# Optimization experiments

Measured on AMD Instinct MI355X. Metric: run time of the kernel, lower is better.

## Reference

```python
import jax, jax.numpy as jnp
import numpy as np

SCALE = 64.0   # CosFace scale s
MARGIN = 0.35  # CosFace margin m
EPS = 1e-12


def setup_inputs() -> dict:
    key = jax.random.key(0)
    k1, k2, k3 = jax.random.split(key, 3)
    batch, feat_dim, num_classes = 512, 512, 100000
    return {
        "input": jax.random.normal(k1, (batch, feat_dim), dtype=jnp.float32),
        "label": jax.random.randint(k2, (batch,), 0, num_classes, dtype=jnp.int64),
        "w": jax.random.normal(k3, (feat_dim, num_classes), dtype=jnp.float32),
    }


def reference(input, label, w):
    # L2-normalize features (rows) and class weights (columns), as in _forward_train
    feat_norm = jnp.clip(jnp.linalg.norm(input, axis=1, keepdims=True), EPS, None)
    normed_feat = input / feat_norm                      # [B, D]
    w_norm = jnp.clip(jnp.linalg.norm(w, axis=0, keepdims=True), EPS, None)
    normed_w = w / w_norm                                # [D, C]
    cosine = jnp.clip(normed_feat @ normed_w, -1.0, 1.0)  # [B, C]
    # CosFace margin applied at the true-label position (get_probs_i)
    onehot = jax.nn.one_hot(label, w.shape[1], dtype=cosine.dtype)
    logits = SCALE * (cosine - MARGIN * onehot)          # [B, C]
    # loss = mean(logsumexp over all (sharded) classes - logit at true label)
    lse = jax.nn.logsumexp(logits, axis=1)               # [B]
    x = jnp.take_along_axis(logits, label[:, None], axis=1)[:, 0]  # [B]
    return jnp.mean(lse - x)
```

## Files before the change

### kernel.cpp

```cpp
#include <hip/hip_runtime.h>
#include <hip/hip_bf16.h>
#include <math.h>

#define BDIM 512
#define DDIM 512
#define CDIM 100000
#define NC 64
#define NCHUNK ((CDIM + NC - 1) / NC)

typedef __attribute__((ext_vector_type(8))) short short8;
typedef __attribute__((ext_vector_type(4))) float f32x4;

__device__ __forceinline__ unsigned short f2bf(float f) {
  unsigned int u = __builtin_bit_cast(unsigned int, f);
  u = (u + 0x7FFFu + ((u >> 16) & 1u)) >> 16;
  return (unsigned short)u;
}

__global__ void k_rownorm(const float* __restrict__ x, unsigned short* __restrict__ a) {
  const int b = blockIdx.x;
  const int tid = threadIdx.x;
  const float* row = x + (size_t)b * DDIM;
  float v0 = row[tid], v1 = row[tid + 256];
  float ss = v0 * v0 + v1 * v1;
  #pragma unroll
  for (int m = 1; m < 64; m <<= 1) ss += __shfl_xor(ss, m);
  __shared__ float sred[4];
  __shared__ float sinv;
  if ((tid & 63) == 0) sred[tid >> 6] = ss;
  __syncthreads();
  if (tid == 0) {
    float s = sred[0] + sred[1] + sred[2] + sred[3];
    sinv = 1.f / fmaxf(sqrtf(s), 1e-12f);
  }
  __syncthreads();
  const float inv = sinv;
  a[(size_t)b * DDIM + tid] = f2bf(v0 * inv);
  a[(size_t)b * DDIM + tid + 256] = f2bf(v1 * inv);
}

__global__ __launch_bounds__(512, 4)
void k_main(const unsigned short* __restrict__ a,
            const float* __restrict__ w,
            const long long* __restrict__ label,
            float2* __restrict__ part,
            float* __restrict__ labellogit) {
  __shared__ __align__(16) unsigned short blds[NC][DDIM];
  __shared__ float ssred[8][NC];
  __shared__ float invwn_sh[NC];

  const int t = threadIdx.x;
  const int chunk = blockIdx.x;
  const int c0 = chunk * NC;
  const bool tailblk = (c0 + NC > CDIM);

  const int wave = t >> 6;
  const int lane = t & 63;
  const int lhi = lane >> 4;
  const int llo = lane & 15;

  const int c4 = (t & 15) * 4;
  const int tg = t >> 4;

  float4 p[16];
  if (!tailblk) {
    #pragma unroll
    for (int h = 0; h < 2; h++)
      #pragma unroll
      for (int j = 0; j < 8; j++) {
        const int k = (tg + 32 * h) * 8 + j;
        p[h * 8 + j] = *reinterpret_cast<const float4*>(w + (size_t)k * CDIM + c0 + c4);
      }
  } else {
    #pragma unroll
    for (int h = 0; h < 2; h++)
      #pragma unroll
      for (int j = 0; j < 8; j++) {
        const int k = (tg + 32 * h) * 8 + j;
        #pragma unroll
        for (int cc = 0; cc < 4; cc++)
          p[h * 8 + j][cc] = (c0 + c4 + cc < CDIM) ? w[(size_t)k * CDIM + c0 + c4 + cc] : 0.f;
      }
  }

  float ss0 = 0.f, ss1 = 0.f, ss2 = 0.f, ss3 = 0.f;
  #pragma unroll
  for (int i = 0; i < 16; i++) {
    ss0 += p[i].x * p[i].x; ss1 += p[i].y * p[i].y;
    ss2 += p[i].z * p[i].z; ss3 += p[i].w * p[i].w;
  }

  #pragma unroll
  for (int h = 0; h < 2; h++) {
    #pragma unroll
    for (int cc = 0; cc < 4; cc++) {
      const int c = c4 + cc;
      short8 v;
      #pragma unroll
      for (int j = 0; j < 8; j++) v[j] = (short)f2bf(p[h * 8 + j][cc]);
      *reinterpret_cast<short8*>(&blds[c][((tg + 32 * h) * 8) ^ ((c & 7) << 3)]) = v;
    }
  }

  #pragma unroll
  for (int msk = 16; msk < 64; msk <<= 1) {
    ss0 += __shfl_xor(ss0, msk);
    ss1 += __shfl_xor(ss1, msk);
    ss2 += __shfl_xor(ss2, msk);
    ss3 += __shfl_xor(ss3, msk);
  }
  if (lane < 16) {
    ssred[wave][c4 + 0] = ss0;
    ssred[wave][c4 + 1] = ss1;
    ssred[wave][c4 + 2] = ss2;
    ssred[wave][c4 + 3] = ss3;
  }
  __syncthreads();
  if (t < NC) {
    float s = 0.f;
    #pragma unroll
    for (int i = 0; i < 8; i++) s += ssred[i][t];
    invwn_sh[t] = 1.f / fmaxf(sqrtf(s), 1e-12f);
  }
  __syncthreads();

  f32x4 acc[4][4];
  #pragma unroll
  for (int i = 0; i < 4; i++)
    #pragma unroll
    for (int j = 0; j < 4; j++)
      acc[i][j] = (f32x4){0.f, 0.f, 0.f, 0.f};

  const unsigned short* ab0 = a + (size_t)(wave * 64 + 0 * 16 + llo) * DDIM + (lhi << 3);
  const unsigned short* ab1 = a + (size_t)(wave * 64 + 1 * 16 + llo) * DDIM + (lhi << 3);
  const unsigned short* ab2 = a + (size_t)(wave * 64 + 2 * 16 + llo) * DDIM + (lhi << 3);
  const unsigned short* ab3 = a + (size_t)(wave * 64 + 3 * 16 + llo) * DDIM + (lhi << 3);

  #pragma unroll
  for (int step = 0; step < 16; step++) {
    const int koff = step * 32;
    short8 af[4], bfr[4];
    af[0] = *reinterpret_cast<const short8*>(ab0 + koff);
    af[1] = *reinterpret_cast<const short8*>(ab1 + koff);
    af[2] = *reinterpret_cast<const short8*>(ab2 + koff);
    af[3] = *reinterpret_cast<const short8*>(ab3 + koff);
    #pragma unroll
    for (int cf = 0; cf < 4; cf++) {
      const int c = cf * 16 + llo;
      bfr[cf] = *reinterpret_cast<const short8*>(
          &blds[c][(koff + (lhi << 3)) ^ ((c & 7) << 3)]);
    }
    #pragma unroll
    for (int rf = 0; rf < 4; rf++)
      #pragma unroll
      for (int cf = 0; cf < 4; cf++)
        acc[rf][cf] = __builtin_amdgcn_mfma_f32_16x16x32_bf16(af[rf], bfr[cf], acc[rf][cf], 0, 0, 0);
  }

  #pragma unroll
  for (int rf = 0; rf < 4; rf++) {
    #pragma unroll
    for (int r = 0; r < 4; r++) {
      const int row = wave * 64 + rf * 16 + (lhi << 2) + r;
      const int lab = (int)label[row];
      float vals[4];
      float mloc = -INFINITY;
      #pragma unroll
      for (int cf = 0; cf < 4; cf++) {
        const int cg = c0 + cf * 16 + llo;
        float cs = acc[rf][cf][r] * invwn_sh[cf * 16 + llo];
        cs = fminf(fmaxf(cs, -1.f), 1.f);
        float lg = 64.f * cs;
        if (cg == lab) { lg = 64.f * (cs - 0.35f); labellogit[row] = lg; }
        if (cg >= CDIM) lg = -INFINITY;
        vals[cf] = lg;
        mloc = fmaxf(mloc, lg);
      }
      float m = mloc;
      #pragma unroll
      for (int msk = 1; msk < 16; msk <<= 1) m = fmaxf(m, __shfl_xor(m, msk));
      float s = 0.f;
      #pragma unroll
      for (int cf = 0; cf < 4; cf++) s += __expf(vals[cf] - m);
      #pragma unroll
      for (int msk = 1; msk < 16; msk <<= 1) s += __shfl_xor(s, msk);
      if (llo == 0) part[(size_t)chunk * BDIM + row] = make_float2(m, s);
    }
  }
}

__global__ void k_rowreduce(const float2* __restrict__ part,
                            const float* __restrict__ labellogit,
                            float* __restrict__ rowloss) {
  const int row = blockIdx.x;
  const int tid = threadIdx.x;
  float m = -INFINITY, s = 0.f;
  for (int ch = tid; ch < NCHUNK; ch += 256) {
    float2 p = part[(size_t)ch * BDIM + row];
    float nm = fmaxf(m, p.x);
    s = s * __expf(m - nm) + p.y * __expf(p.x - nm);
    m = nm;
  }
  #pragma unroll
  for (int msk = 1; msk < 64; msk <<= 1) {
    float om = __shfl_xor(m, msk), os = __shfl_xor(s, msk);
    float nm = fmaxf(m, om);
    s = s * __expf(m - nm) + os * __expf(om - nm);
    m = nm;
  }
  __shared__ float sm[4], ssum[4];
  const int wv = tid >> 6, ln = tid & 63;
  if (ln == 0) { sm[wv] = m; ssum[wv] = s; }
  __syncthreads();
  if (tid == 0) {
    float M = sm[0], S = ssum[0];
    #pragma unroll
    for (int i = 1; i < 4; i++) {
      float nm = fmaxf(M, sm[i]);
      S = S * __expf(M - nm) + ssum[i] * __expf(sm[i] - nm);
      M = nm;
    }
    rowloss[row] = M + logf(S) - labellogit[row];
  }
}

__global__ void k_mean(const float* __restrict__ rowloss, float* __restrict__ out) {
  const int tid = threadIdx.x;
  float v = rowloss[tid];
  #pragma unroll
  for (int msk = 1; msk < 64; msk <<= 1) v += __shfl_xor(v, msk);
  __shared__ float sred[8];
  if ((tid & 63) == 0) sred[tid >> 6] = v;
  __syncthreads();
  if (tid == 0) {
    float s = 0.f;
    #pragma unroll
    for (int i = 0; i < 8; i++) s += sred[i];
    out[0] = s / (float)BDIM;
  }
}

extern "C" void kernel_launch(void* const* d_in, const int* in_sizes, int n_in,
                              void* d_out, int out_size, void* d_ws, size_t ws_size,
                              hipStream_t stream) {
  const float* input = (const float*)d_in[0];
  const long long* label = (const long long*)d_in[1];
  const float* w = (const float*)d_in[2];
  float* out = (float*)d_out;

  char* ws = (char*)d_ws;
  unsigned short* a_bf16 = (unsigned short*)ws;
  float2* part = (float2*)(ws + 512 * 1024);
  float* labellogit = (float*)(ws + 512 * 1024 + (size_t)BDIM * NCHUNK * sizeof(float2));
  float* rowloss = labellogit + BDIM;

  k_rownorm<<<BDIM, 256, 0, stream>>>(input, a_bf16);
  k_main<<<NCHUNK, 512, 0, stream>>>(a_bf16, w, label, part, labellogit);
  k_rowreduce<<<BDIM, 256, 0, stream>>>(part, labellogit, rowloss);
  k_mean<<<1, BDIM, 0, stream>>>(rowloss, out);
}
```

Before: 173.1 us.

## Pre-transpose W to bf16 with column norms, then stream tiles via global_load_lds

Adds a separate kernel that reads the fp32 weight matrix once. It transposes it through shared memory into a column-major bf16 copy in workspace and computes the inverse column norms there. The main GEMM kernel no longer converts or reduces fp32 weights. It loads each 64-column tile straight into swizzled LDS with direct global-to-LDS loads and reads the precomputed norms. This removes the strided fp32 loads and conversion from the MFMA kernel, at the cost of an extra bf16 write and re-read of the whole weight matrix and one more launch.

```diff
diff --git a/kernel.cpp b/kernel.cpp
--- a/kernel.cpp
+++ b/kernel.cpp
@@ -7,6 +7,8 @@
 #define CDIM 100000
 #define NC 64
 #define NCHUNK ((CDIM + NC - 1) / NC)
+#define CPAD (NCHUNK * NC)
+#define CTILE 128
 
 typedef __attribute__((ext_vector_type(8))) short short8;
 typedef __attribute__((ext_vector_type(4))) float f32x4;
@@ -15,6 +17,12 @@
   unsigned int u = __builtin_bit_cast(unsigned int, f);
   u = (u + 0x7FFFu + ((u >> 16) & 1u)) >> 16;
   return (unsigned short)u;
+}
+
+__device__ __forceinline__ void gl_lds16(const unsigned short* g, unsigned short* l) {
+  __builtin_amdgcn_global_load_lds(
+      (const __attribute__((address_space(1))) void*)g,
+      (__attribute__((address_space(3))) void*)l, 16, 0, 0);
 }
 
 __global__ void k_rownorm(const float* __restrict__ x, unsigned short* __restrict__ a) {
@@ -39,89 +47,87 @@
   a[(size_t)b * DDIM + tid + 256] = f2bf(v1 * inv);
 }
 
+__global__ __launch_bounds__(512)
+void k_wt(const float* __restrict__ w, unsigned short* __restrict__ wt,
+          float* __restrict__ invwn) {
+  __shared__ float tile[64][CTILE + 4];
+  const int t = threadIdx.x;
+  const int c0w = blockIdx.x * CTILE;
+  const int rd_d = t >> 3;
+  const int rd_c = (t & 7) * 16;
+  const int wc = t >> 2;
+  const int wh = t & 3;
+  float ss = 0.f;
+
+  for (int ch = 0; ch < 8; ch++) {
+    const int d0 = ch * 64;
+    float4 r[4];
+    #pragma unroll
+    for (int j = 0; j < 4; j++) {
+      const int c = c0w + rd_c + j * 4;
+      if (c < CDIM)
+        r[j] = *reinterpret_cast<const float4*>(w + (size_t)(d0 + rd_d) * CDIM + c);
+      else
+        r[j] = (float4){0.f, 0.f, 0.f, 0.f};
+    }
+    #pragma unroll
+    for (int j = 0; j < 4; j++)
+      *reinterpret_cast<float4*>(&tile[rd_d][rd_c + j * 4]) = r[j];
+    __syncthreads();
+
+    short8 o0, o1;
+    #pragma unroll
+    for (int j = 0; j < 8; j++) {
+      const float v = tile[wh * 16 + j][wc];
+      ss += v * v;
+      o0[j] = (short)f2bf(v);
+    }
+    #pragma unroll
+    for (int j = 0; j < 8; j++) {
+      const float v = tile[wh * 16 + 8 + j][wc];
+      ss += v * v;
+      o1[j] = (short)f2bf(v);
+    }
+    if (c0w + wc < CDIM) {
+      unsigned short* dst = wt + ((size_t)(c0w + wc) << 9) + d0 + wh * 16;
+      *reinterpret_cast<short8*>(dst) = o0;
+      *reinterpret_cast<short8*>(dst + 8) = o1;
+    }
+    __syncthreads();
+  }
+  ss += __shfl_xor(ss, 1);
+  ss += __shfl_xor(ss, 2);
+  if (wh == 0 && c0w + wc < CDIM)
+    invwn[c0w + wc] = 1.f / fmaxf(sqrtf(ss), 1e-12f);
+}
+
 __global__ __launch_bounds__(512, 4)
 void k_main(const unsigned short* __restrict__ a,
-            const float* __restrict__ w,
+            const unsigned short* __restrict__ wt,
+            const float* __restrict__ invwn,
             const long long* __restrict__ label,
             float2* __restrict__ part,
             float* __restrict__ labellogit) {
   __shared__ __align__(16) unsigned short blds[NC][DDIM];
-  __shared__ float ssred[8][NC];
   __shared__ float invwn_sh[NC];
 
   const int t = threadIdx.x;
   const int chunk = blockIdx.x;
   const int c0 = chunk * NC;
-  const bool tailblk = (c0 + NC > CDIM);
 
   const int wave = t >> 6;
   const int lane = t & 63;
   const int lhi = lane >> 4;
   const int llo = lane & 15;
 
-  const int c4 = (t & 15) * 4;
-  const int tg = t >> 4;
-
-  float4 p[16];
-  if (!tailblk) {
-    #pragma unroll
-    for (int h = 0; h < 2; h++)
-      #pragma unroll
-      for (int j = 0; j < 8; j++) {
-        const int k = (tg + 32 * h) * 8 + j;
-        p[h * 8 + j] = *reinterpret_cast<const float4*>(w + (size_t)k * CDIM + c0 + c4);
-      }
-  } else {
-    #pragma unroll
-    for (int h = 0; h < 2; h++)
-      #pragma unroll
-      for (int j = 0; j < 8; j++) {
-        const int k = (tg + 32 * h) * 8 + j;
-        #pragma unroll
-        for (int cc = 0; cc < 4; cc++)
-          p[h * 8 + j][cc] = (c0 + c4 + cc < CDIM) ? w[(size_t)k * CDIM + c0 + c4 + cc] : 0.f;
-      }
-  }
-
-  float ss0 = 0.f, ss1 = 0.f, ss2 = 0.f, ss3 = 0.f;
-  #pragma unroll
-  for (int i = 0; i < 16; i++) {
-    ss0 += p[i].x * p[i].x; ss1 += p[i].y * p[i].y;
-    ss2 += p[i].z * p[i].z; ss3 += p[i].w * p[i].w;
-  }
-
-  #pragma unroll
-  for (int h = 0; h < 2; h++) {
-    #pragma unroll
-    for (int cc = 0; cc < 4; cc++) {
-      const int c = c4 + cc;
-      short8 v;
-      #pragma unroll
-      for (int j = 0; j < 8; j++) v[j] = (short)f2bf(p[h * 8 + j][cc]);
-      *reinterpret_cast<short8*>(&blds[c][((tg + 32 * h) * 8) ^ ((c & 7) << 3)]) = v;
-    }
-  }
-
-  #pragma unroll
-  for (int msk = 16; msk < 64; msk <<= 1) {
-    ss0 += __shfl_xor(ss0, msk);
-    ss1 += __shfl_xor(ss1, msk);
-    ss2 += __shfl_xor(ss2, msk);
-    ss3 += __shfl_xor(ss3, msk);
-  }
-  if (lane < 16) {
-    ssred[wave][c4 + 0] = ss0;
-    ssred[wave][c4 + 1] = ss1;
-    ssred[wave][c4 + 2] = ss2;
-    ssred[wave][c4 + 3] = ss3;
-  }
-  __syncthreads();
-  if (t < NC) {
-    float s = 0.f;
-    #pragma unroll
-    for (int i = 0; i < 8; i++) s += ssred[i][t];
-    invwn_sh[t] = 1.f / fmaxf(sqrtf(s), 1e-12f);
-  }
+  if (t < NC) invwn_sh[t] = invwn[c0 + t];
+
+  #pragma unroll
+  for (int i = 0; i < 8; i++) {
+    const int c = wave * 8 + i;
+    gl_lds16(wt + ((size_t)(c0 + c) << 9) + ((lane ^ i) << 3), &blds[c][0]);
+  }
+  asm volatile("s_waitcnt vmcnt(0)" ::: "memory");
   __syncthreads();
 
   f32x4 acc[4][4];
@@ -249,13 +255,16 @@
   float* out = (float*)d_out;
 
   char* ws = (char*)d_ws;
-  unsigned short* a_bf16 = (unsigned short*)ws;
-  float2* part = (float2*)(ws + 512 * 1024);
-  float* labellogit = (float*)(ws + 512 * 1024 + (size_t)BDIM * NCHUNK * sizeof(float2));
-  float* rowloss = labellogit + BDIM;
+  unsigned short* a_bf16 = (unsigned short*)(ws + 0);
+  float2* part           = (float2*)(ws + 524288);
+  float* labellogit      = (float*)(ws + 6926336);
+  float* rowloss         = (float*)(ws + 6928384);
+  float* invwn           = (float*)(ws + 6930432);
+  unsigned short* w_t    = (unsigned short*)(ws + 7330560);
 
   k_rownorm<<<BDIM, 256, 0, stream>>>(input, a_bf16);
-  k_main<<<NCHUNK, 512, 0, stream>>>(a_bf16, w, label, part, labellogit);
+  k_wt<<<(CDIM + CTILE - 1) / CTILE, 512, 0, stream>>>(w, w_t, invwn);
+  k_main<<<NCHUNK, 512, 0, stream>>>(a_bf16, w_t, invwn, label, part, labellogit);
   k_rowreduce<<<BDIM, 256, 0, stream>>>(part, labellogit, rowloss);
   k_mean<<<1, BDIM, 0, stream>>>(rowloss, out);
 }
```

New measurement: 248.5 us. 1.44x slower.

## Warp-specialize main kernel into persistent producer/consumer with double-buffered LDS

Applied to the files above, without the earlier changes.

Turns the one-chunk-per-block GEMM+softmax kernel into a persistent kernel with 256 blocks of 1024 threads. Eight producer waves load and convert W chunks to bf16 into a double-buffered LDS tile and compute column norms, while eight consumer waves run MFMA and the per-chunk logsumexp on the other buffer. The goal is to overlap the HBM streaming of W with the matrix math and epilogue. In exchange it uses twice the LDS, needs a block barrier per chunk, and runs a single 1024-thread block per CU, which lowers occupancy.

```diff
diff --git a/kernel.cpp b/kernel.cpp
--- a/kernel.cpp
+++ b/kernel.cpp
@@ -7,6 +7,7 @@
 #define CDIM 100000
 #define NC 64
 #define NCHUNK ((CDIM + NC - 1) / NC)
+#define GRID 256
 
 typedef __attribute__((ext_vector_type(8))) short short8;
 typedef __attribute__((ext_vector_type(4))) float f32x4;
@@ -39,152 +40,171 @@
   a[(size_t)b * DDIM + tid + 256] = f2bf(v1 * inv);
 }
 
-__global__ __launch_bounds__(512, 4)
+__global__ __launch_bounds__(1024, 4)
 void k_main(const unsigned short* __restrict__ a,
             const float* __restrict__ w,
             const long long* __restrict__ label,
             float2* __restrict__ part,
             float* __restrict__ labellogit) {
-  __shared__ __align__(16) unsigned short blds[NC][DDIM];
-  __shared__ float ssred[8][NC];
-  __shared__ float invwn_sh[NC];
+  __shared__ __align__(16) unsigned short blds[2][NC][DDIM];
+  __shared__ float ssred[2][8][NC];
 
   const int t = threadIdx.x;
-  const int chunk = blockIdx.x;
-  const int c0 = chunk * NC;
-  const bool tailblk = (c0 + NC > CDIM);
-
-  const int wave = t >> 6;
-  const int lane = t & 63;
-  const int lhi = lane >> 4;
-  const int llo = lane & 15;
-
-  const int c4 = (t & 15) * 4;
-  const int tg = t >> 4;
-
-  float4 p[16];
-  if (!tailblk) {
-    #pragma unroll
-    for (int h = 0; h < 2; h++)
-      #pragma unroll
-      for (int j = 0; j < 8; j++) {
-        const int k = (tg + 32 * h) * 8 + j;
-        p[h * 8 + j] = *reinterpret_cast<const float4*>(w + (size_t)k * CDIM + c0 + c4);
-      }
+  const int bid = blockIdx.x;
+  const int nloc = (NCHUNK - bid + GRID - 1) / GRID;
+
+  if (t >= 512) {
+    const int tp = t - 512;
+    const int pw = tp >> 6;
+    const int lane = tp & 63;
+    const int c4 = (tp & 15) * 4;
+    const int tg = tp >> 4;
+    float4 p[16];
+
+    auto issue = [&](int sq) {
+      const int chunk = bid + sq * GRID;
+      const int c0 = chunk * NC;
+      const bool tail = (c0 + NC > CDIM);
+      #pragma unroll
+      for (int h = 0; h < 2; h++)
+        #pragma unroll
+        for (int j = 0; j < 8; j++) {
+          const int k = (tg + 32 * h) * 8 + j;
+          const float* src = w + (size_t)k * CDIM + c0 + c4;
+          if (!tail) {
+            p[h * 8 + j] = *reinterpret_cast<const float4*>(src);
+          } else {
+            #pragma unroll
+            for (int cc = 0; cc < 4; cc++)
+              p[h * 8 + j][cc] = (c0 + c4 + cc < CDIM) ? src[cc] : 0.f;
+          }
+        }
+    };
+    auto commit = [&](int sq) {
+      const int buf = sq & 1;
+      float ss0 = 0.f, ss1 = 0.f, ss2 = 0.f, ss3 = 0.f;
+      #pragma unroll
+      for (int i = 0; i < 16; i++) {
+        ss0 += p[i].x * p[i].x; ss1 += p[i].y * p[i].y;
+        ss2 += p[i].z * p[i].z; ss3 += p[i].w * p[i].w;
+      }
+      #pragma unroll
+      for (int h = 0; h < 2; h++)
+        #pragma unroll
+        for (int cc = 0; cc < 4; cc++) {
+          const int c = c4 + cc;
+          short8 v;
+          #pragma unroll
+          for (int j = 0; j < 8; j++) v[j] = (short)f2bf(p[h * 8 + j][cc]);
+          *reinterpret_cast<short8*>(
+              &blds[buf][c][((tg + 32 * h) * 8) ^ ((c & 7) << 3)]) = v;
+        }
+      #pragma unroll
+      for (int msk = 16; msk < 64; msk <<= 1) {
+        ss0 += __shfl_xor(ss0, msk);
+        ss1 += __shfl_xor(ss1, msk);
+        ss2 += __shfl_xor(ss2, msk);
+        ss3 += __shfl_xor(ss3, msk);
+      }
+      if (lane < 16)
+        *reinterpret_cast<float4*>(&ssred[buf][pw][c4]) = (float4){ss0, ss1, ss2, ss3};
+    };
+
+    issue(0);
+    commit(0);
+    if (nloc > 1) issue(1);
+    __syncthreads();
+    for (int sq = 0; sq < nloc; sq++) {
+      if (sq + 1 < nloc) commit(sq + 1);
+      if (sq + 2 < nloc) issue(sq + 2);
+      __syncthreads();
+    }
   } else {
-    #pragma unroll
-    for (int h = 0; h < 2; h++)
-      #pragma unroll
-      for (int j = 0; j < 8; j++) {
-        const int k = (tg + 32 * h) * 8 + j;
-        #pragma unroll
-        for (int cc = 0; cc < 4; cc++)
-          p[h * 8 + j][cc] = (c0 + c4 + cc < CDIM) ? w[(size_t)k * CDIM + c0 + c4 + cc] : 0.f;
-      }
-  }
-
-  float ss0 = 0.f, ss1 = 0.f, ss2 = 0.f, ss3 = 0.f;
-  #pragma unroll
-  for (int i = 0; i < 16; i++) {
-    ss0 += p[i].x * p[i].x; ss1 += p[i].y * p[i].y;
-    ss2 += p[i].z * p[i].z; ss3 += p[i].w * p[i].w;
-  }
-
-  #pragma unroll
-  for (int h = 0; h < 2; h++) {
-    #pragma unroll
-    for (int cc = 0; cc < 4; cc++) {
-      const int c = c4 + cc;
-      short8 v;
-      #pragma unroll
-      for (int j = 0; j < 8; j++) v[j] = (short)f2bf(p[h * 8 + j][cc]);
-      *reinterpret_cast<short8*>(&blds[c][((tg + 32 * h) * 8) ^ ((c & 7) << 3)]) = v;
-    }
-  }
-
-  #pragma unroll
-  for (int msk = 16; msk < 64; msk <<= 1) {
-    ss0 += __shfl_xor(ss0, msk);
-    ss1 += __shfl_xor(ss1, msk);
-    ss2 += __shfl_xor(ss2, msk);
-    ss3 += __shfl_xor(ss3, msk);
-  }
-  if (lane < 16) {
-    ssred[wave][c4 + 0] = ss0;
-    ssred[wave][c4 + 1] = ss1;
-    ssred[wave][c4 + 2] = ss2;
-    ssred[wave][c4 + 3] = ss3;
-  }
-  __syncthreads();
-  if (t < NC) {
-    float s = 0.f;
-    #pragma unroll
-    for (int i = 0; i < 8; i++) s += ssred[i][t];
-    invwn_sh[t] = 1.f / fmaxf(sqrtf(s), 1e-12f);
-  }
-  __syncthreads();
-
-  f32x4 acc[4][4];
-  #pragma unroll
-  for (int i = 0; i < 4; i++)
-    #pragma unroll
-    for (int j = 0; j < 4; j++)
-      acc[i][j] = (f32x4){0.f, 0.f, 0.f, 0.f};
-
-  const unsigned short* ab0 = a + (size_t)(wave * 64 + 0 * 16 + llo) * DDIM + (lhi << 3);
-  const unsigned short* ab1 = a + (size_t)(wave * 64 + 1 * 16 + llo) * DDIM + (lhi << 3);
-  const unsigned short* ab2 = a + (size_t)(wave * 64 + 2 * 16 + llo) * DDIM + (lhi << 3);
-  const unsigned short* ab3 = a + (size_t)(wave * 64 + 3 * 16 + llo) * DDIM + (lhi << 3);
-
-  #pragma unroll
-  for (int step = 0; step < 16; step++) {
-    const int koff = step * 32;
-    short8 af[4], bfr[4];
-    af[0] = *reinterpret_cast<const short8*>(ab0 + koff);
-    af[1] = *reinterpret_cast<const short8*>(ab1 + koff);
-    af[2] = *reinterpret_cast<const short8*>(ab2 + koff);
-    af[3] = *reinterpret_cast<const short8*>(ab3 + koff);
-    #pragma unroll
-    for (int cf = 0; cf < 4; cf++) {
-      const int c = cf * 16 + llo;
-      bfr[cf] = *reinterpret_cast<const short8*>(
-          &blds[c][(koff + (lhi << 3)) ^ ((c & 7) << 3)]);
-    }
-    #pragma unroll
-    for (int rf = 0; rf < 4; rf++)
-      #pragma unroll
-      for (int cf = 0; cf < 4; cf++)
-        acc[rf][cf] = __builtin_amdgcn_mfma_f32_16x16x32_bf16(af[rf], bfr[cf], acc[rf][cf], 0, 0, 0);
-  }
-
-  #pragma unroll
-  for (int rf = 0; rf < 4; rf++) {
-    #pragma unroll
-    for (int r = 0; r < 4; r++) {
-      const int row = wave * 64 + rf * 16 + (lhi << 2) + r;
-      const int lab = (int)label[row];
-      float vals[4];
-      float mloc = -INFINITY;
+    const int wave = t >> 6;
+    const int lane = t & 63;
+    const int lhi = lane >> 4;
+    const int llo = lane & 15;
+
+    const unsigned short* ab0 = a + (size_t)(wave * 64 + 0 * 16 + llo) * DDIM + (lhi << 3);
+    const unsigned short* ab1 = a + (size_t)(wave * 64 + 1 * 16 + llo) * DDIM + (lhi << 3);
+    const unsigned short* ab2 = a + (size_t)(wave * 64 + 2 * 16 + llo) * DDIM + (lhi << 3);
+    const unsigned short* ab3 = a + (size_t)(wave * 64 + 3 * 16 + llo) * DDIM + (lhi << 3);
+
+    __syncthreads();
+    for (int sq = 0; sq < nloc; sq++) {
+      const int chunk = bid + sq * GRID;
+      const int c0 = chunk * NC;
+      const int buf = sq & 1;
+
+      f32x4 acc[4][4];
+      #pragma unroll
+      for (int i = 0; i < 4; i++)
+        #pragma unroll
+        for (int j = 0; j < 4; j++)
+          acc[i][j] = (f32x4){0.f, 0.f, 0.f, 0.f};
+
+      #pragma unroll
+      for (int step = 0; step < 16; step++) {
+        const int koff = step * 32;
+        short8 af[4], bfr[4];
+        af[0] = *reinterpret_cast<const short8*>(ab0 + koff);
+        af[1] = *reinterpret_cast<const short8*>(ab1 + koff);
+        af[2] = *reinterpret_cast<const short8*>(ab2 + koff);
+        af[3] = *reinterpret_cast<const short8*>(ab3 + koff);
+        #pragma unroll
+        for (int cf = 0; cf < 4; cf++) {
+          const int c = cf * 16 + llo;
+          bfr[cf] = *reinterpret_cast<const short8*>(
+              &blds[buf][c][(koff + (lhi << 3)) ^ ((c & 7) << 3)]);
+        }
+        #pragma unroll
+        for (int rf = 0; rf < 4; rf++)
+          #pragma unroll
+          for (int cf = 0; cf < 4; cf++)
+            acc[rf][cf] = __builtin_amdgcn_mfma_f32_16x16x32_bf16(af[rf], bfr[cf], acc[rf][cf], 0, 0, 0);
+      }
+
+      float inv[4];
       #pragma unroll
       for (int cf = 0; cf < 4; cf++) {
-        const int cg = c0 + cf * 16 + llo;
-        float cs = acc[rf][cf][r] * invwn_sh[cf * 16 + llo];
-        cs = fminf(fmaxf(cs, -1.f), 1.f);
-        float lg = 64.f * cs;
-        if (cg == lab) { lg = 64.f * (cs - 0.35f); labellogit[row] = lg; }
-        if (cg >= CDIM) lg = -INFINITY;
-        vals[cf] = lg;
-        mloc = fmaxf(mloc, lg);
-      }
-      float m = mloc;
-      #pragma unroll
-      for (int msk = 1; msk < 16; msk <<= 1) m = fmaxf(m, __shfl_xor(m, msk));
-      float s = 0.f;
-      #pragma unroll
-      for (int cf = 0; cf < 4; cf++) s += __expf(vals[cf] - m);
-      #pragma unroll
-      for (int msk = 1; msk < 16; msk <<= 1) s += __shfl_xor(s, msk);
-      if (llo == 0) part[(size_t)chunk * BDIM + row] = make_float2(m, s);
+        const int c = cf * 16 + llo;
+        float s = 0.f;
+        #pragma unroll
+        for (int pw = 0; pw < 8; pw++) s += ssred[buf][pw][c];
+        inv[cf] = 1.f / fmaxf(sqrtf(s), 1e-12f);
+      }
+
+      #pragma unroll
+      for (int rf = 0; rf < 4; rf++) {
+        #pragma unroll
+        for (int r = 0; r < 4; r++) {
+          const int row = wave * 64 + rf * 16 + (lhi << 2) + r;
+          const int lab = (int)label[row];
+          float vals[4];
+          float mloc = -INFINITY;
+          #pragma unroll
+          for (int cf = 0; cf < 4; cf++) {
+            const int cg = c0 + cf * 16 + llo;
+            float cs = acc[rf][cf][r] * inv[cf];
+            cs = fminf(fmaxf(cs, -1.f), 1.f);
+            float lg = 64.f * cs;
+            if (cg == lab) { lg = 64.f * (cs - 0.35f); labellogit[row] = lg; }
+            if (cg >= CDIM) lg = -INFINITY;
+            vals[cf] = lg;
+            mloc = fmaxf(mloc, lg);
+          }
+          float m = mloc;
+          #pragma unroll
+          for (int msk = 1; msk < 16; msk <<= 1) m = fmaxf(m, __shfl_xor(m, msk));
+          float s = 0.f;
+          #pragma unroll
+          for (int cf = 0; cf < 4; cf++) s += __expf(vals[cf] - m);
+          #pragma unroll
+          for (int msk = 1; msk < 16; msk <<= 1) s += __shfl_xor(s, msk);
+          if (llo == 0) part[(size_t)chunk * BDIM + row] = make_float2(m, s);
+        }
+      }
+      __syncthreads();
     }
   }
 }
@@ -249,13 +269,13 @@
   float* out = (float*)d_out;
 
   char* ws = (char*)d_ws;
-  unsigned short* a_bf16 = (unsigned short*)ws;
-  float2* part = (float2*)(ws + 512 * 1024);
-  float* labellogit = (float*)(ws + 512 * 1024 + (size_t)BDIM * NCHUNK * sizeof(float2));
-  float* rowloss = labellogit + BDIM;
+  unsigned short* a_bf16 = (unsigned short*)(ws + 0);
+  float2* part           = (float2*)(ws + 524288);
+  float* labellogit      = (float*)(ws + 6926336);
+  float* rowloss         = (float*)(ws + 6928384);
 
   k_rownorm<<<BDIM, 256, 0, stream>>>(input, a_bf16);
-  k_main<<<NCHUNK, 512, 0, stream>>>(a_bf16, w, label, part, labellogit);
+  k_main<<<GRID, 1024, 0, stream>>>(a_bf16, w, label, part, labellogit);
   k_rowreduce<<<BDIM, 256, 0, stream>>>(part, labellogit, rowloss);
   k_mean<<<1, BDIM, 0, stream>>>(rowloss, out);
 }
```

Result: slower. 356.9 us (+106.2%).
